# Optimization experiments

Measured on AMD Instinct MI355X. Metric: run time of the kernel, lower is better.

The kernel has to match this reference:

```python
import jax, jax.numpy as jnp
import numpy as np

OUT, IN = 4096, 4096  # W_shape
K, BLOCK = 256, 8     # codebook entries, block dim


def setup_inputs() -> dict:
    key = jax.random.key(0)
    k1, k2, k3, k4, k5 = jax.random.split(key, 5)
    x = jax.random.normal(k1, (4, 2048, IN), dtype=jnp.float32)
    centroids = jax.random.normal(k2, (K, BLOCK), dtype=jnp.float32)
    labels = jax.random.randint(k3, (OUT * IN // BLOCK,), 0, K, dtype=jnp.int64)
    scale = jax.random.uniform(k4, (IN,), dtype=jnp.float32)
    bias = jax.random.normal(k5, (OUT,), dtype=jnp.float32)
    return {"x": x, "centroids": centroids, "labels": labels, "scale": scale, "bias": bias}


def reference(x, centroids, labels, scale, bias):
    # VQ weight decompression: gather codebook vectors, reshape to [OUT, IN]
    W_smooth = centroids[labels].reshape(OUT, IN)
    # F.linear(x * scale, W, bias) == (x*scale) @ W.T + bias
    return jnp.einsum('bsi,oi->bso', x * scale, W_smooth) + bias
```

## Files before the change

### kernel.cpp

```cpp
#include <hip/hip_runtime.h>
#include <stdint.h>

#define M_DIM 8192
#define N_DIM 4096
#define K_DIM 4096
#define NUM_VQ (N_DIM * K_DIM / 8)
#define NUM_X  (M_DIM * K_DIM)
#define VQ_BLOCKS (NUM_VQ / 256)
#define CVT_BLOCKS (NUM_X / 8 / 256)

typedef __attribute__((ext_vector_type(4))) float f32x4;
typedef __attribute__((ext_vector_type(8))) short bf16x8;
typedef unsigned short u16;

__device__ inline unsigned short f2bf(float f) {
    union { float f; unsigned int i; } v; v.f = f;
    unsigned int x = v.i;
    return (unsigned short)((x + 0x7FFFu + ((x >> 16) & 1u)) >> 16);
}

__global__ void detect_i64(const int* __restrict__ labels, int* __restrict__ flag) {
    int v = labels[2 * threadIdx.x + 1];
    unsigned long long nz = __ballot(v != 0);
    if (threadIdx.x == 0) *flag = (nz == 0ull) ? 1 : 0;
}

__global__ void prep(const int* __restrict__ labels,
                     const float* __restrict__ centroids,
                     const float* __restrict__ scale,
                     const float* __restrict__ x,
                     u16* __restrict__ Ws, u16* __restrict__ Xb,
                     const int* __restrict__ flag) {
    int b = blockIdx.x;
    if (b < VQ_BLOCKS) {
        int i = b * 256 + threadIdx.x;
        int lab = (*flag) ? labels[2 * i] : labels[i];
        int kb = i & 511;
        f32x4 c0 = ((const f32x4*)centroids)[2 * lab];
        f32x4 c1 = ((const f32x4*)centroids)[2 * lab + 1];
        f32x4 s0 = ((const f32x4*)scale)[2 * kb];
        f32x4 s1 = ((const f32x4*)scale)[2 * kb + 1];
        bf16x8 o;
#pragma unroll
        for (int j = 0; j < 4; ++j) {
            o[j]     = (short)f2bf(c0[j] * s0[j]);
            o[4 + j] = (short)f2bf(c1[j] * s1[j]);
        }
        ((bf16x8*)Ws)[i] = o;
    } else {
        int i = (b - VQ_BLOCKS) * 256 + threadIdx.x;
        f32x4 a = ((const f32x4*)x)[2 * i];
        f32x4 c = ((const f32x4*)x)[2 * i + 1];
        bf16x8 o;
#pragma unroll
        for (int j = 0; j < 4; ++j) { o[j] = (short)f2bf(a[j]); o[4 + j] = (short)f2bf(c[j]); }
        ((bf16x8*)Xb)[i] = o;
    }
}

__global__ __launch_bounds__(256)
void gemm_bias(const u16* __restrict__ A, const u16* __restrict__ B,
               const float* __restrict__ bias, float* __restrict__ C) {
    __shared__ u16 ldsA[128 * 32];
    __shared__ u16 ldsB[128 * 32];

    const int tid  = threadIdx.x;
    const int wave = tid >> 6;
    const int lane = tid & 63;
    const int bm = blockIdx.y * 128;
    const int bn = blockIdx.x * 128;

    const int srow = wave * 32 + (lane >> 2);
    const int scol = (((lane & 3) ^ ((lane >> 3) & 3))) * 8;
    const u16* gA = A + (size_t)(bm + srow) * K_DIM + scol;
    const u16* gB = B + (size_t)(bn + srow) * K_DIM + scol;
    u16* lA = ldsA + wave * 1024;
    u16* lB = ldsB + wave * 1024;

    const int wm = (wave >> 1) * 64;
    const int wn = (wave & 1) * 64;
    const int fm = lane & 15;
    const int fks = (((lane >> 4) ^ ((lane >> 1) & 3)) & 3) * 8;

    f32x4 acc[4][4];
#pragma unroll
    for (int i = 0; i < 4; ++i)
#pragma unroll
        for (int j = 0; j < 4; ++j)
            acc[i][j] = (f32x4){0.f, 0.f, 0.f, 0.f};

    for (int kt = 0; kt < K_DIM / 32; ++kt) {
        __builtin_amdgcn_global_load_lds(
            (const __attribute__((address_space(1))) void*)gA,
            (__attribute__((address_space(3))) void*)lA, 16, 0, 0);
        __builtin_amdgcn_global_load_lds(
            (const __attribute__((address_space(1))) void*)(gA + 16 * K_DIM),
            (__attribute__((address_space(3))) void*)(lA + 512), 16, 0, 0);
        __builtin_amdgcn_global_load_lds(
            (const __attribute__((address_space(1))) void*)gB,
            (__attribute__((address_space(3))) void*)lB, 16, 0, 0);
        __builtin_amdgcn_global_load_lds(
            (const __attribute__((address_space(1))) void*)(gB + 16 * K_DIM),
            (__attribute__((address_space(3))) void*)(lB + 512), 16, 0, 0);
        gA += 32;
        gB += 32;
        __syncthreads();

        bf16x8 af[4], bfr[4];
#pragma unroll
        for (int i = 0; i < 4; ++i)
            af[i] = *(const bf16x8*)&ldsA[(wm + i * 16 + fm) * 32 + fks];
#pragma unroll
        for (int j = 0; j < 4; ++j)
            bfr[j] = *(const bf16x8*)&ldsB[(wn + j * 16 + fm) * 32 + fks];

#pragma unroll
        for (int i = 0; i < 4; ++i)
#pragma unroll
            for (int j = 0; j < 4; ++j)
                acc[i][j] = __builtin_amdgcn_mfma_f32_16x16x32_bf16(
                    af[i], bfr[j], acc[i][j], 0, 0, 0);
        __syncthreads();
    }

    float biasv[4];
#pragma unroll
    for (int j = 0; j < 4; ++j)
        biasv[j] = bias[bn + wn + j * 16 + (lane & 15)];

    const int crow0 = bm + wm + (lane >> 4) * 4;
    const int ccol0 = bn + wn + (lane & 15);
#pragma unroll
    for (int i = 0; i < 4; ++i)
#pragma unroll
        for (int r = 0; r < 4; ++r) {
            size_t rowoff = (size_t)(crow0 + i * 16 + r) * N_DIM;
#pragma unroll
            for (int j = 0; j < 4; ++j)
                C[rowoff + ccol0 + j * 16] = acc[i][j][r] + biasv[j];
        }
}

extern "C" void kernel_launch(void* const* d_in, const int* in_sizes, int n_in,
                              void* d_out, int out_size, void* d_ws, size_t ws_size,
                              hipStream_t stream) {
    const float* x         = (const float*)d_in[0];
    const float* centroids = (const float*)d_in[1];
    const int*   labels    = (const int*)d_in[2];
    const float* scale     = (const float*)d_in[3];
    const float* bias      = (const float*)d_in[4];
    float* out             = (float*)d_out;

    int* flag = (int*)d_ws;
    u16* Ws   = (u16*)((char*)d_ws + 256);
    u16* Xb   = (u16*)((char*)d_ws + 256 + (size_t)NUM_VQ * 16);

    detect_i64<<<1, 64, 0, stream>>>(labels, flag);
    prep<<<VQ_BLOCKS + CVT_BLOCKS, 256, 0, stream>>>(labels, centroids, scale, x,
                                                     Ws, Xb, flag);

    dim3 grid(N_DIM / 128, M_DIM / 128);
    gemm_bias<<<grid, 256, 0, stream>>>(Xb, Ws, bias, out);
}
```

Baseline: 538.9 us.

## Warp-specialize GEMM with producer waves and 4-stage LDS ring buffer

```diff
diff --git a/kernel.cpp b/kernel.cpp
--- a/kernel.cpp
+++ b/kernel.cpp
@@ -9,6 +9,13 @@
 #define VQ_BLOCKS (NUM_VQ / 256)
 #define CVT_BLOCKS (NUM_X / 8 / 256)
 
+#define DEPTH  4
+#define TILES  (K_DIM / 32)
+#define ROUNDS (TILES / DEPTH)
+
+#define AS1 __attribute__((address_space(1)))
+#define AS3 __attribute__((address_space(3)))
+
 typedef __attribute__((ext_vector_type(4))) float f32x4;
 typedef __attribute__((ext_vector_type(8))) short bf16x8;
 typedef unsigned short u16;
@@ -19,22 +26,18 @@
     return (unsigned short)((x + 0x7FFFu + ((x >> 16) & 1u)) >> 16);
 }
 
-__global__ void detect_i64(const int* __restrict__ labels, int* __restrict__ flag) {
-    int v = labels[2 * threadIdx.x + 1];
-    unsigned long long nz = __ballot(v != 0);
-    if (threadIdx.x == 0) *flag = (nz == 0ull) ? 1 : 0;
-}
-
 __global__ void prep(const int* __restrict__ labels,
                      const float* __restrict__ centroids,
                      const float* __restrict__ scale,
                      const float* __restrict__ x,
-                     u16* __restrict__ Ws, u16* __restrict__ Xb,
-                     const int* __restrict__ flag) {
+                     u16* __restrict__ Ws, u16* __restrict__ Xb) {
     int b = blockIdx.x;
     if (b < VQ_BLOCKS) {
+        int lane = threadIdx.x & 63;
+        int probe = labels[2 * lane + 1];
+        bool is64 = (__ballot(probe != 0) == 0ull);
         int i = b * 256 + threadIdx.x;
-        int lab = (*flag) ? labels[2 * i] : labels[i];
+        int lab = is64 ? labels[2 * i] : labels[i];
         int kb = i & 511;
         f32x4 c0 = ((const f32x4*)centroids)[2 * lab];
         f32x4 c1 = ((const f32x4*)centroids)[2 * lab + 1];
@@ -58,11 +61,12 @@
     }
 }
 
-__global__ __launch_bounds__(256)
+__global__ __launch_bounds__(512, 4)
 void gemm_bias(const u16* __restrict__ A, const u16* __restrict__ B,
                const float* __restrict__ bias, float* __restrict__ C) {
-    __shared__ u16 ldsA[128 * 32];
-    __shared__ u16 ldsB[128 * 32];
+    __shared__ u16 buf[DEPTH * 8192];
+    __shared__ int ready[DEPTH];
+    __shared__ int done[DEPTH];
 
     const int tid  = threadIdx.x;
     const int wave = tid >> 6;
@@ -70,12 +74,42 @@
     const int bm = blockIdx.y * 128;
     const int bn = blockIdx.x * 128;
 
-    const int srow = wave * 32 + (lane >> 2);
-    const int scol = (((lane & 3) ^ ((lane >> 3) & 3))) * 8;
-    const u16* gA = A + (size_t)(bm + srow) * K_DIM + scol;
-    const u16* gB = B + (size_t)(bn + srow) * K_DIM + scol;
-    u16* lA = ldsA + wave * 1024;
-    u16* lB = ldsB + wave * 1024;
+    if (tid < DEPTH) done[tid] = 0;
+    else if (tid < 2 * DEPTH) ready[tid - DEPTH] = 0;
+    __syncthreads();
+
+    if (wave >= 4) {
+        const int s = wave - 4;
+        u16* stA = buf + s * 8192;
+        u16* stB = stA + 4096;
+        const int prow = lane >> 2;
+        const int scol = (((lane & 3) ^ ((lane >> 3) & 3))) * 8;
+        const u16* baseA = A + (size_t)(bm + prow) * K_DIM + scol;
+        const u16* baseB = B + (size_t)(bn + prow) * K_DIM + scol;
+
+        for (int r = 0; r < ROUNDS; ++r) {
+            const int kt = r * DEPTH + s;
+            while (__hip_atomic_load(&done[s], __ATOMIC_ACQUIRE,
+                                     __HIP_MEMORY_SCOPE_WORKGROUP) < 4 * r)
+                __builtin_amdgcn_s_sleep(1);
+            const u16* gA = baseA + kt * 32;
+            const u16* gB = baseB + kt * 32;
+#pragma unroll
+            for (int j = 0; j < 8; ++j)
+                __builtin_amdgcn_global_load_lds(
+                    (const AS1 void*)(gA + (size_t)(16 * j) * K_DIM),
+                    (AS3 void*)(stA + j * 512), 16, 0, 0);
+#pragma unroll
+            for (int j = 0; j < 8; ++j)
+                __builtin_amdgcn_global_load_lds(
+                    (const AS1 void*)(gB + (size_t)(16 * j) * K_DIM),
+                    (AS3 void*)(stB + j * 512), 16, 0, 0);
+            asm volatile("s_waitcnt vmcnt(0)" ::: "memory");
+            __hip_atomic_store(&ready[s], r + 1, __ATOMIC_RELEASE,
+                               __HIP_MEMORY_SCOPE_WORKGROUP);
+        }
+        return;
+    }
 
     const int wm = (wave >> 1) * 64;
     const int wn = (wave & 1) * 64;
@@ -89,30 +123,26 @@
         for (int j = 0; j < 4; ++j)
             acc[i][j] = (f32x4){0.f, 0.f, 0.f, 0.f};
 
-    for (int kt = 0; kt < K_DIM / 32; ++kt) {
-        __builtin_amdgcn_global_load_lds(
-            (const __attribute__((address_space(1))) void*)gA,
-            (__attribute__((address_space(3))) void*)lA, 16, 0, 0);
-        __builtin_amdgcn_global_load_lds(
-            (const __attribute__((address_space(1))) void*)(gA + 16 * K_DIM),
-            (__attribute__((address_space(3))) void*)(lA + 512), 16, 0, 0);
-        __builtin_amdgcn_global_load_lds(
-            (const __attribute__((address_space(1))) void*)gB,
-            (__attribute__((address_space(3))) void*)lB, 16, 0, 0);
-        __builtin_amdgcn_global_load_lds(
-            (const __attribute__((address_space(1))) void*)(gB + 16 * K_DIM),
-            (__attribute__((address_space(3))) void*)(lB + 512), 16, 0, 0);
-        gA += 32;
-        gB += 32;
-        __syncthreads();
+    for (int kt = 0; kt < TILES; ++kt) {
+        const int s = kt & (DEPTH - 1);
+        const int r = kt >> 2;
+        while (__hip_atomic_load(&ready[s], __ATOMIC_ACQUIRE,
+                                 __HIP_MEMORY_SCOPE_WORKGROUP) < r + 1)
+            __builtin_amdgcn_s_sleep(1);
+        const u16* stA = buf + s * 8192;
+        const u16* stB = stA + 4096;
 
         bf16x8 af[4], bfr[4];
 #pragma unroll
         for (int i = 0; i < 4; ++i)
-            af[i] = *(const bf16x8*)&ldsA[(wm + i * 16 + fm) * 32 + fks];
+            af[i] = *(const bf16x8*)&stA[(wm + i * 16 + fm) * 32 + fks];
 #pragma unroll
         for (int j = 0; j < 4; ++j)
-            bfr[j] = *(const bf16x8*)&ldsB[(wn + j * 16 + fm) * 32 + fks];
+            bfr[j] = *(const bf16x8*)&stB[(wn + j * 16 + fm) * 32 + fks];
+
+        if (lane == 0)
+            __hip_atomic_fetch_add(&done[s], 1, __ATOMIC_RELEASE,
+                                   __HIP_MEMORY_SCOPE_WORKGROUP);
 
 #pragma unroll
         for (int i = 0; i < 4; ++i)
@@ -120,7 +150,6 @@
             for (int j = 0; j < 4; ++j)
                 acc[i][j] = __builtin_amdgcn_mfma_f32_16x16x32_bf16(
                     af[i], bfr[j], acc[i][j], 0, 0, 0);
-        __syncthreads();
     }
 
     float biasv[4];
@@ -151,14 +180,12 @@
     const float* bias      = (const float*)d_in[4];
     float* out             = (float*)d_out;
 
-    int* flag = (int*)d_ws;
-    u16* Ws   = (u16*)((char*)d_ws + 256);
-    u16* Xb   = (u16*)((char*)d_ws + 256 + (size_t)NUM_VQ * 16);
+    u16* Ws = (u16*)d_ws;
+    u16* Xb = (u16*)((char*)d_ws + (size_t)NUM_VQ * 16);
 
-    detect_i64<<<1, 64, 0, stream>>>(labels, flag);
     prep<<<VQ_BLOCKS + CVT_BLOCKS, 256, 0, stream>>>(labels, centroids, scale, x,
-                                                     Ws, Xb, flag);
+                                                     Ws, Xb);
 
     dim3 grid(N_DIM / 128, M_DIM / 128);
-    gemm_bias<<<grid, 256, 0, stream>>>(Xb, Ws, bias, out);
+    gemm_bias<<<grid, 512, 0, stream>>>(Xb, Ws, bias, out);
 }
```

Result: faster. 525.4 us (-2.5%).
